# Performance work log

Hardware: AMD Instinct MI355X
Metric: run time of the kernel (lower is better)

The kernel has to match this reference:

```python
import jax, jax.numpy as jnp
import numpy as np
from jax import lax

L = 2        # encoder layers
D = 256      # d_model
H = 8        # nhead
DH = D // H  # head dim
CF = 2       # compression_factor (default in CustomizedAttn)
FF = 2048    # dim_feedforward
B = 10       # batch (forced: null_k has shape (10,1,D))
HH = 40
WW = 40
T = HH * WW  # seq len = 1600
EPS = 1e-5


def setup_inputs() -> dict:
    key = jax.random.key(0)
    ks = jax.random.split(key, 16)
    f = lambda k, shp: jax.random.normal(k, shp, jnp.float32) * 0.02
    return {
        "src": jax.random.normal(ks[0], (B, D, HH, WW), jnp.float32),
        "pos_embed": jax.random.normal(ks[1], (B, D, HH, WW), jnp.float32),
        "Wq": f(ks[2], (L, D, D)),
        "Wk": f(ks[3], (L, D, D)),
        "Wv": f(ks[4], (L, D, D)),
        "Wo": f(ks[5], (L, D, D)),
        "bo": jnp.zeros((L, D), jnp.float32),
        "conv_w": f(ks[6], (L, D, D // H, CF)),  # grouped Conv1d weight [out, in/groups, k]
        "conv_b": jnp.zeros((L, D), jnp.float32),
        "null_k": f(ks[7], (L, B, 1, D)),
        "null_v": f(ks[8], (L, B, 1, D)),
        "ln1_g": jnp.ones((L, D), jnp.float32),
        "ln1_b": jnp.zeros((L, D), jnp.float32),
        "ln2_g": jnp.ones((L, D), jnp.float32),
        "ln2_b": jnp.zeros((L, D), jnp.float32),
        "W1": f(ks[9], (L, FF, D)),
        "b1": jnp.zeros((L, FF), jnp.float32),
        "W2": f(ks[10], (L, D, FF)),
        "b2": jnp.zeros((L, D), jnp.float32),
    }


def _layernorm(x, g, b):
    m = jnp.mean(x, axis=-1, keepdims=True)
    v = jnp.var(x, axis=-1, keepdims=True)
    return (x - m) * lax.rsqrt(v + EPS) * g + b


def _attn(x, pos, Wq, Wk, Wv, Wo, bo, cw, cb, nk, nv):
    # x, pos: [B, T, D]
    qk = x + pos
    q = qk @ Wq.T
    k = qk @ Wk.T
    v = x @ Wv.T
    # torch: padding = cf - t % cf -> always in [1, cf], so padding ALWAYS applied
    pad = CF - (T % CF)
    k = jnp.pad(k, ((0, 0), (pad, 0), (0, 0)))
    v = jnp.pad(v, ((0, 0), (pad, 0), (0, 0)))

    def compress(t_):  # grouped strided Conv1d over time, shared weights for k and v
        y = lax.conv_general_dilated(
            t_.transpose(0, 2, 1), cw, (CF,), "VALID",
            dimension_numbers=("NCH", "OIH", "NCH"), feature_group_count=H)
        return (y + cb[None, :, None]).transpose(0, 2, 1)

    k = jnp.concatenate([nk, compress(k)], axis=1)  # [B, Tc+10, D]
    v = jnp.concatenate([nv, compress(v)], axis=1)
    split = lambda t_: t_.reshape(B, t_.shape[1], H, DH).transpose(0, 2, 1, 3)
    qh, kh, vh = split(q), split(k), split(v)
    # NOTE: scale uses FULL d_model (d ** -0.5), faithful to the source.
    dots = jnp.einsum("bhid,bhjd->bhij", qh, kh) * (D ** -0.5)
    # NOTE: the source computes softmax(dots) but then overwrites it with
    # dropout(dots); at inference attention weights are the raw scaled dots.
    out = jnp.einsum("bhij,bhjd->bhid", dots, vh)
    out = out.transpose(0, 2, 1, 3).reshape(B, T, D)
    return out @ Wo.T + bo


def reference(src, pos_embed, Wq, Wk, Wv, Wo, bo, conv_w, conv_b, null_k, null_v,
              ln1_g, ln1_b, ln2_g, ln2_b, W1, b1, W2, b2):
    x = src.reshape(B, D, T).transpose(0, 2, 1)        # [B, T, D]
    pos = pos_embed.reshape(B, D, T).transpose(0, 2, 1)
    for l in range(L):
        a = _attn(x, pos, Wq[l], Wk[l], Wv[l], Wo[l], bo[l],
                  conv_w[l], conv_b[l], null_k[l], null_v[l])
        x = _layernorm(x + a, ln1_g[l], ln1_b[l])
        ff = jnp.maximum(x @ W1[l].T + b1[l], 0.0) @ W2[l].T + b2[l]
        x = _layernorm(x + ff, ln2_g[l], ln2_b[l])
    return x.transpose(0, 2, 1).reshape(B, D, HH, WW)
```

## Files before the change

kernel.cpp:

```cpp
#include <hip/hip_runtime.h>
#include <math.h>

typedef __attribute__((ext_vector_type(8))) short short8;
typedef __attribute__((ext_vector_type(4))) short short4v;
typedef __attribute__((ext_vector_type(4))) float f32x4;
typedef unsigned int u32;

constexpr int Bsz = 10;
constexpr int Dm  = 256;
constexpr int Hh  = 8;
constexpr int Tt  = 1600;
constexpr int FFd = 2048;
constexpr int Tkv = 802;
constexpr int JCH = 8;
constexpr size_t Fsz  = (size_t)Bsz * Tt * Dm;
constexpr size_t PAD  = 65536;
constexpr size_t KVsz = (size_t)Bsz * Tkv * Dm;
constexpr size_t FHsz = (size_t)Bsz * Tt * FFd;
constexpr size_t WBsz = 2621440;

__device__ float g_x[Fsz];
__device__ float g_qk[Fsz];
__device__ float g_t[Fsz];
__device__ float g_kc[KVsz];
__device__ float g_vc[KVsz];
__device__ float g_kvm[(size_t)Bsz * Hh * 32 * 32];
__device__ float g_kvp[(size_t)JCH * Bsz * Hh * 32 * 32];
__device__ float g_pos[Fsz];
__device__ unsigned short g_xb[Fsz + PAD];
__device__ unsigned short g_qkb[Fsz + PAD];
__device__ unsigned short g_tb[Fsz + PAD];
__device__ unsigned short g_qb[Fsz + PAD];
__device__ __attribute__((aligned(16))) unsigned short g_ffh[FHsz + PAD];
__device__ unsigned short g_wb[WBsz];
__device__ unsigned short g_wo2[(size_t)Bsz * Dm * Dm];

__device__ __forceinline__ float* selbuf(int id) {
  switch (id) {
    case 0: return g_x;
    case 1: return g_qk;
    case 2: return g_t;
    case 3: return g_kc;
    case 4: return g_vc;
    case 5: return g_kvm;
    case 6: return (float*)g_ffh;
    default: return (float*)g_ffh + Fsz;
  }
}
__device__ __forceinline__ unsigned short* selbufb(int id) {
  switch (id) {
    case 0: return g_xb;
    case 1: return g_qkb;
    case 2: return g_tb;
    case 3: return g_ffh;
    default: return g_qb;
  }
}

__device__ __forceinline__ unsigned short f2b(float x) {
  unsigned int u = __float_as_uint(x);
  u += 0x7FFFu + ((u >> 16) & 1u);
  return (unsigned short)(u >> 16);
}
__device__ __forceinline__ float b2f(unsigned short u) {
  return __uint_as_float(((unsigned int)u) << 16);
}

__global__ __launch_bounds__(256) void wconv_all_k(
    const float* __restrict__ Wk, const float* __restrict__ Wq,
    const float* __restrict__ Wv, const float* __restrict__ Wo,
    const float* __restrict__ W1, const float* __restrict__ W2) {
  const int i = blockIdx.x * 256 + threadIdx.x;
  float v;
  if (i < 262144) {
    const int l = i >> 17, r = i & 131071;
    v = (r < 65536) ? Wk[l * 65536 + r] : Wq[l * 65536 + (r - 65536)];
  } else if (i < 393216) {
    v = Wv[i - 262144];
  } else if (i < 524288) {
    v = Wo[i - 393216];
  } else if (i < 1572864) {
    v = W1[i - 524288];
  } else {
    v = W2[i - 1572864];
  }
  g_wb[i] = f2b(v);
}

__global__ __launch_bounds__(256) void trans_in2_k(const float* __restrict__ src,
                                                   const float* __restrict__ pose) {
  __shared__ float ts[32][33];
  __shared__ float tp[32][33];
  const int tx = threadIdx.x & 31, ty = threadIdx.x >> 5;
  const int t0 = blockIdx.x * 32, d0 = blockIdx.y * 32, b = blockIdx.z;
  #pragma unroll
  for (int i = ty; i < 32; i += 8) {
    const size_t gi = ((size_t)(b * Dm + d0 + i)) * Tt + t0 + tx;
    ts[i][tx] = src[gi];
    tp[i][tx] = pose[gi];
  }
  __syncthreads();
  #pragma unroll
  for (int i = ty; i < 32; i += 8) {
    const size_t idx = ((size_t)(b * Tt + t0 + i)) * Dm + d0 + tx;
    const float s = ts[tx][i], p = tp[tx][i];
    g_x[idx] = s;
    g_pos[idx] = p;
    g_xb[idx] = f2b(s);
    g_qkb[idx] = f2b(s + p);
  }
}

__global__ __launch_bounds__(256) void trans_out_k(float* out) {
  __shared__ float tile[32][33];
  const int tx = threadIdx.x & 31, ty = threadIdx.x >> 5;
  const int t0 = blockIdx.x * 32, d0 = blockIdx.y * 32, b = blockIdx.z;
  #pragma unroll
  for (int i = ty; i < 32; i += 8)
    tile[i][tx] = g_x[((size_t)(b * Tt + t0 + i)) * Dm + d0 + tx];
  __syncthreads();
  #pragma unroll
  for (int i = ty; i < 32; i += 8)
    out[((size_t)(b * Dm + d0 + i)) * Tt + t0 + tx] = tile[tx][i];
}

template<int BN, bool DUAL, bool PERB, bool RELU, bool BIAS, bool CBF16>
__global__ __launch_bounds__(256) void gemm2_k(
    int Aid, int woff, const float* __restrict__ bias, int Cid, int C2id,
    int NB, int M, int N, int K) {
  constexpr int BM = 128, BK = 64;
  constexpr int ACH = BM * 8;
  constexpr int BCH = BN * 8;
  constexpr int NW = BN / 32;
  __shared__ short8 As8[3][ACH];
  __shared__ short8 Bs8[3][BCH];
  const int tid = threadIdx.x;
  const int lane = tid & 63, wid = tid >> 6;
  const int wr = wid >> 1, wc = wid & 1;

  const int nwg = gridDim.x;
  const int bid = blockIdx.x;
  const int q = nwg >> 3, r = nwg & 7;
  const int xcd = bid & 7, seq = bid >> 3;
  const int wgid = (xcd < r ? xcd * (q + 1) : r * (q + 1) + (xcd - r) * q) + seq;

  int m0, n0, mlim;
  const unsigned short* W16;
  if constexpr (PERB) {
    const int per = 13 * NB;
    const int b = wgid / per;
    const int rem = wgid - b * per;
    m0 = b * Tt + (rem / NB) * BM;
    n0 = (rem % NB) * BN;
    mlim = b * Tt + Tt;
    W16 = g_wo2 + (size_t)b * 65536;
  } else {
    m0 = (wgid / NB) * BM;
    n0 = (wgid % NB) * BN;
    mlim = M;
    W16 = g_wb + woff;
  }

  const unsigned short* A16 = selbufb(Aid);
  const bool second = DUAL && (n0 >= 256);
  float* Cf = selbuf(second ? C2id : Cid);
  unsigned short* C16 = selbufb(second ? C2id : Cid);
  const int gn0 = second ? n0 - 256 : n0;
  const int cstride = DUAL ? 256 : N;

  f32x4 acc[4][NW];
  #pragma unroll
  for (int m = 0; m < 4; ++m)
    #pragma unroll
    for (int n = 0; n < NW; ++n) acc[m][n] = (f32x4){0.f, 0.f, 0.f, 0.f};

  const int lkc = lane >> 4, lrc = lane & 15;

  auto stage = [&](int t, int buf) {
    const int k0 = t * BK;
    #pragma unroll
    for (int i = 0; i < ACH / 256; ++i) {
      const int c = tid + i * 256;
      const int row = c >> 3, kc = c & 7;
      const unsigned short* gs = A16 + (size_t)(m0 + row) * K + k0 +
                                 ((kc ^ (row & 7)) << 3);
      __builtin_amdgcn_global_load_lds(
          (const __attribute__((address_space(1))) u32*)gs,
          (__attribute__((address_space(3))) u32*)&As8[buf][c], 16, 0, 0);
    }
    #pragma unroll
    for (int i = 0; i < BCH / 256; ++i) {
      const int c = tid + i * 256;
      const int row = c >> 3, kc = c & 7;
      const unsigned short* gs = W16 + (size_t)(n0 + row) * K + k0 +
                                 ((kc ^ (row & 7)) << 3);
      __builtin_amdgcn_global_load_lds(
          (const __attribute__((address_space(1))) u32*)gs,
          (__attribute__((address_space(3))) u32*)&Bs8[buf][c], 16, 0, 0);
    }
  };

  const int nt = K / BK;
  stage(0, 0);
  if (nt > 1) stage(1, 1);
  int cur = 0, nxt = 2;
  for (int t = 0; t < nt; ++t) {
    if (t + 1 < nt) {
      asm volatile("s_waitcnt vmcnt(6)" ::: "memory");
    } else {
      asm volatile("s_waitcnt vmcnt(0)" ::: "memory");
    }
    __builtin_amdgcn_sched_barrier(0);
    __builtin_amdgcn_s_barrier();
    __builtin_amdgcn_sched_barrier(0);
    if (t + 2 < nt) stage(t + 2, nxt);
    #pragma unroll
    for (int kk = 0; kk < 2; ++kk) {
      short8 af[4], bf[NW];
      #pragma unroll
      for (int m = 0; m < 4; ++m) {
        const int r2 = wr * 64 + m * 16 + lrc;
        af[m] = As8[cur][r2 * 8 + ((kk * 4 + lkc) ^ (r2 & 7))];
      }
      #pragma unroll
      for (int n = 0; n < NW; ++n) {
        const int cn = wc * (BN / 2) + n * 16 + lrc;
        bf[n] = Bs8[cur][cn * 8 + ((kk * 4 + lkc) ^ (cn & 7))];
      }
      #pragma unroll
      for (int m = 0; m < 4; ++m)
        #pragma unroll
        for (int n = 0; n < NW; ++n)
          acc[m][n] = __builtin_amdgcn_mfma_f32_16x16x32_bf16(
              af[m], bf[n], acc[m][n], 0, 0, 0);
    }
    cur = (cur == 2) ? 0 : cur + 1;
    nxt = (nxt == 2) ? 0 : nxt + 1;
  }

  constexpr int CSTR = (BN == 64) ? BN + 4 : BN;
  float* ldsC = (float*)&As8[0][0];
  {
    asm volatile("s_waitcnt vmcnt(0)" ::: "memory");
    __builtin_amdgcn_s_barrier();
    const int r0 = lkc * 4;
    #pragma unroll
    for (int m = 0; m < 4; ++m)
      #pragma unroll
      for (int n = 0; n < NW; ++n) {
        const int col = wc * (BN / 2) + n * 16 + lrc;
        #pragma unroll
        for (int j = 0; j < 4; ++j)
          ldsC[(wr * 64 + m * 16 + r0 + j) * CSTR + col] = acc[m][n][j];
      }
    __syncthreads();
  }
  if constexpr (CBF16) {
    constexpr int CH = BM * BN / 8;
    #pragma unroll
    for (int i = 0; i < CH / 256; ++i) {
      const int c = tid + i * 256;
      const int rowl = c / (BN / 8), col8 = (c % (BN / 8)) * 8;
      if (PERB && m0 + rowl >= mlim) continue;
      short8 v;
      #pragma unroll
      for (int j = 0; j < 8; ++j) {
        float x = ldsC[rowl * CSTR + col8 + j];
        if (BIAS) x += bias[gn0 + col8 + j];
        if (RELU) x = fmaxf(x, 0.f);
        v[j] = (short)f2b(x);
      }
      *(short8*)(C16 + (size_t)(m0 + rowl) * cstride + gn0 + col8) = v;
    }
  } else {
    constexpr int CH = BM * BN / 4;
    #pragma unroll
    for (int i = 0; i < CH / 256; ++i) {
      const int c = tid + i * 256;
      const int rowl = c / (BN / 4), col4 = (c % (BN / 4)) * 4;
      if (PERB && m0 + rowl >= mlim) continue;
      float4 v;
      float* pv = &v.x;
      #pragma unroll
      for (int j = 0; j < 4; ++j) {
        float x = ldsC[rowl * CSTR + col4 + j];
        if (BIAS) x += bias[gn0 + col4 + j];
        if (RELU) x = fmaxf(x, 0.f);
        pv[j] = x;
      }
      *(float4*)(Cf + (size_t)(m0 + rowl) * cstride + gn0 + col4) = v;
    }
  }
}

__global__ __launch_bounds__(512, 1) void gemmf_k(
    int Aid, int w1off, int w2off, const float* __restrict__ b1p,
    const float* __restrict__ b2p) {
  constexpr int BM = 128, NCH = 16;
  __shared__ short8 ws[4096];
  __shared__ short8 h8[512];
  __shared__ float b1f[512];
  const int tid = threadIdx.x;
  const int lane = tid & 63, wid = tid >> 6;
  const int lkc = lane >> 4, lrc = lane & 15;
  const int nwg = gridDim.x, bid = blockIdx.x;
  const int q = nwg >> 3, r = nwg & 7;
  const int xcd = bid & 7, seq = bid >> 3;
  const int wgid = (xcd < r ? xcd * (q + 1) : r * (q + 1) + (xcd - r) * q) + seq;
  const int qd = wgid / 125;
  const int m0 = (wgid - qd * 125) * BM;
  const int hb = qd * 512;
  const unsigned short* A16 = selbufb(Aid);
  const unsigned short* W1p = g_wb + w1off;
  const unsigned short* W2p = g_wb + w2off;
  float* Cf;
  if (qd == 0) Cf = g_qk;
  else if (qd == 1) Cf = g_t;
  else Cf = (float*)g_ffh + (size_t)(qd - 2) * Fsz;

  #pragma unroll
  for (int i = 0; i < 8; ++i) {
    const int c = tid + i * 512;
    const int row = c >> 5, kc = c & 31;
    const unsigned short* gs = A16 + (size_t)(m0 + row) * 256 +
                               ((kc ^ (row & 31)) << 3);
    __builtin_amdgcn_global_load_lds(
        (const __attribute__((address_space(1))) u32*)gs,
        (__attribute__((address_space(3))) u32*)&ws[c], 16, 0, 0);
  }
  __builtin_amdgcn_global_load_lds(
      (const __attribute__((address_space(1))) u32*)(b1p + hb + tid),
      (__attribute__((address_space(3))) u32*)&b1f[tid], 4, 0, 0);
  asm volatile("s_waitcnt vmcnt(0)" ::: "memory");
  __builtin_amdgcn_sched_barrier(0);
  __builtin_amdgcn_s_barrier();

  const int mg = wid >> 1, ng = wid & 1;
  short8 areg[2][8];
  #pragma unroll
  for (int m = 0; m < 2; ++m)
    #pragma unroll
    for (int s = 0; s < 8; ++s) {
      const int r2 = mg * 32 + m * 16 + lrc;
      areg[m][s] = ws[r2 * 32 + ((s * 4 + lkc) ^ (r2 & 31))];
    }
  asm volatile("s_waitcnt lgkmcnt(0)" ::: "memory");
  __builtin_amdgcn_sched_barrier(0);
  __builtin_amdgcn_s_barrier();

  auto stage_w = [&](int ch, int buf) {
    const int kb = hb + ch * 32;
    #pragma unroll
    for (int i = 0; i < 2; ++i) {
      const int c = tid + i * 512;
      const int row = c >> 5, kc = c & 31;
      const unsigned short* gs = W1p + (size_t)(kb + row) * 256 +
                                 ((kc ^ (row & 31)) << 3);
      __builtin_amdgcn_global_load_lds(
          (const __attribute__((address_space(1))) u32*)gs,
          (__attribute__((address_space(3))) u32*)&ws[buf * 2048 + c], 16, 0, 0);
    }
    #pragma unroll
    for (int i = 0; i < 2; ++i) {
      const int c = tid + i * 512;
      const int row = c >> 2, kc = c & 3;
      const int g = (kc ^ (row & 3) ^ ((row >> 2) & 3)) & 3;
      const unsigned short* gs = W2p + (size_t)row * 2048 + kb + (g << 3);
      __builtin_amdgcn_global_load_lds(
          (const __attribute__((address_space(1))) u32*)gs,
          (__attribute__((address_space(3))) u32*)&ws[buf * 2048 + 1024 + c],
          16, 0, 0);
    }
  };
  stage_w(0, 0);

  const int wr = wid >> 2, wc = wid & 3;
  f32x4 acc2[4][4];
  #pragma unroll
  for (int m = 0; m < 4; ++m)
    #pragma unroll
    for (int n = 0; n < 4; ++n) acc2[m][n] = (f32x4){0.f, 0.f, 0.f, 0.f};

  for (int ch = 0; ch < NCH; ++ch) {
    const int cur = ch & 1;
    const int wb = cur * 2048;
    asm volatile("s_waitcnt vmcnt(0)" ::: "memory");
    __builtin_amdgcn_sched_barrier(0);
    __builtin_amdgcn_s_barrier();
    __builtin_amdgcn_sched_barrier(0);
    if (ch + 1 < NCH) stage_w(ch + 1, cur ^ 1);

    f32x4 a1[2];
    a1[0] = (f32x4){0.f, 0.f, 0.f, 0.f};
    a1[1] = (f32x4){0.f, 0.f, 0.f, 0.f};
    const int cn1 = ng * 16 + lrc;
    #pragma unroll
    for (int s = 0; s < 8; ++s) {
      short8 bf = ws[wb + cn1 * 32 + ((s * 4 + lkc) ^ cn1)];
      a1[0] = __builtin_amdgcn_mfma_f32_16x16x32_bf16(areg[0][s], bf, a1[0], 0, 0, 0);
      a1[1] = __builtin_amdgcn_mfma_f32_16x16x32_bf16(areg[1][s], bf, a1[1], 0, 0, 0);
    }
    unsigned short* h16 = (unsigned short*)h8;
    #pragma unroll
    for (int m = 0; m < 2; ++m)
      #pragma unroll
      for (int j = 0; j < 4; ++j) {
        const int row = mg * 32 + m * 16 + lkc * 4 + j;
        const float v = fmaxf(a1[m][j] + b1f[ch * 32 + cn1], 0.f);
        const int g = ((cn1 >> 3) ^ (row & 3) ^ ((row >> 2) & 3)) & 3;
        h16[row * 32 + g * 8 + (cn1 & 7)] = f2b(v);
      }
    asm volatile("s_waitcnt lgkmcnt(0)" ::: "memory");
    __builtin_amdgcn_sched_barrier(0);
    __builtin_amdgcn_s_barrier();
    __builtin_amdgcn_sched_barrier(0);

    short8 af2[4], bf2[4];
    #pragma unroll
    for (int m = 0; m < 4; ++m) {
      const int r2 = wr * 64 + m * 16 + lrc;
      af2[m] = h8[r2 * 4 + ((lkc ^ (r2 & 3) ^ ((r2 >> 2) & 3)) & 3)];
    }
    #pragma unroll
    for (int n = 0; n < 4; ++n) {
      const int cn = wc * 64 + n * 16 + lrc;
      bf2[n] = ws[wb + 1024 + cn * 4 + ((lkc ^ (cn & 3) ^ ((cn >> 2) & 3)) & 3)];
    }
    #pragma unroll
    for (int m = 0; m < 4; ++m)
      #pragma unroll
      for (int n = 0; n < 4; ++n)
        acc2[m][n] = __builtin_amdgcn_mfma_f32_16x16x32_bf16(
            af2[m], bf2[n], acc2[m][n], 0, 0, 0);
  }

  const int r0 = lkc * 4;
  #pragma unroll
  for (int m = 0; m < 4; ++m) {
    const int gm = m0 + wr * 64 + m * 16 + r0;
    #pragma unroll
    for (int n = 0; n < 4; ++n) {
      const int gn = wc * 64 + n * 16 + lrc;
      const float bb = (qd == 0) ? b2p[gn] : 0.f;
      #pragma unroll
      for (int j = 0; j < 4; ++j)
        Cf[(size_t)(gm + j) * 256 + gn] = acc2[m][n][j] + bb;
    }
  }
}

__global__ __launch_bounds__(256) void compress2_k(
    const float* __restrict__ cw, const float* __restrict__ cb,
    const float* __restrict__ nk, const float* __restrict__ nv) {
  __shared__ float rows[32][256];
  const int tc0 = 1 + blockIdx.x * 16;
  const int b = blockIdx.y;
  const int z = blockIdx.z;
  const int tid = threadIdx.x;
  const int o = tid;
  const int g = o >> 5;

  const unsigned short* srcbuf = z ? g_ffh : g_tb;
  const float* nul = z ? nv : nk;
  float* outb = (z ? g_vc : g_kc) + (size_t)b * Tkv * Dm;

  const int r0g = 2 * tc0 - 2;
  const unsigned short* src = srcbuf + ((size_t)b * Tt + r0g) * Dm;
  #pragma unroll
  for (int i = 0; i < 4; ++i) {
    const int c = tid + i * 256;
    const int row = c >> 5, off = (c & 31) * 8;
    short8 v = *(const short8*)(src + (size_t)row * 256 + off);
    #pragma unroll
    for (int j = 0; j < 8; ++j)
      rows[row][off + j] = b2f((unsigned short)v[j]);
  }

  float we[32], wo[32];
  {
    const float4* wp = (const float4*)(cw + o * 64);
    #pragma unroll
    for (int i = 0; i < 16; ++i) {
      float4 w4 = wp[i];
      we[i * 2 + 0] = w4.x; wo[i * 2 + 0] = w4.y;
      we[i * 2 + 1] = w4.z; wo[i * 2 + 1] = w4.w;
    }
  }
  const float bias = cb[o];
  if (blockIdx.x == 0) {
    outb[o] = nul[b * Dm + o];
    outb[Dm + o] = bias;
  }
  __syncthreads();

  float* outp = outb + o;
  #pragma unroll
  for (int t = 0; t < 16; ++t) {
    const int lr = 2 * t;
    const float* p0 = &rows[lr][g * 32];
    const float* p1 = &rows[lr + 1][g * 32];
    float acc = bias;
    #pragma unroll
    for (int i4 = 0; i4 < 8; ++i4) {
      float4 a0 = *(const float4*)(p0 + i4 * 4);
      float4 a1 = *(const float4*)(p1 + i4 * 4);
      acc = fmaf(we[i4 * 4 + 0], a0.x, acc);
      acc = fmaf(we[i4 * 4 + 1], a0.y, acc);
      acc = fmaf(we[i4 * 4 + 2], a0.z, acc);
      acc = fmaf(we[i4 * 4 + 3], a0.w, acc);
      acc = fmaf(wo[i4 * 4 + 0], a1.x, acc);
      acc = fmaf(wo[i4 * 4 + 1], a1.y, acc);
      acc = fmaf(wo[i4 * 4 + 2], a1.z, acc);
      acc = fmaf(wo[i4 * 4 + 3], a1.w, acc);
    }
    outp[(size_t)(1 + tc0 + t) * Dm] = acc;
  }
}

__global__ __launch_bounds__(256) void kvout1_k() {
  __shared__ float kl[8][32];
  __shared__ float vl[8][32];
  const int bh = blockIdx.x;
  const int js = blockIdx.y;
  const int b = bh >> 3, h = bh & 7;
  const int j0 = js * 101;
  const int jend = (j0 + 101 < Tkv) ? j0 + 101 : Tkv;

  const int tid = threadIdx.x;
  const int lr = tid >> 5;
  const int lc = tid & 31;
  const int e = tid >> 3;
  const int d0 = (tid & 7) * 4;

  float a0 = 0.f, a1 = 0.f, a2 = 0.f, a3 = 0.f;
  const size_t base = (size_t)b * Tkv * Dm + h * 32;

  for (int jc = j0; jc < jend; jc += 8) {
    const int jr = jc + lr;
    if (jr < jend) {
      kl[lr][lc] = g_kc[base + (size_t)jr * Dm + lc];
      vl[lr][lc] = g_vc[base + (size_t)jr * Dm + lc];
    } else {
      kl[lr][lc] = 0.f;
      vl[lr][lc] = 0.f;
    }
    __syncthreads();
    #pragma unroll
    for (int r = 0; r < 8; ++r) {
      const float kf = kl[r][e];
      const float* vr = &vl[r][d0];
      a0 = fmaf(kf, vr[0], a0);
      a1 = fmaf(kf, vr[1], a1);
      a2 = fmaf(kf, vr[2], a2);
      a3 = fmaf(kf, vr[3], a3);
    }
    __syncthreads();
  }
  float* op = g_kvp + ((size_t)js * 80 + bh) * 1024 + e * 32 + d0;
  op[0] = a0; op[1] = a1; op[2] = a2; op[3] = a3;
}

__global__ __launch_bounds__(256) void kvout2_k() {
  const int bh = blockIdx.x;
  const int tid = threadIdx.x;
  const int e = tid >> 3;
  const int d0 = (tid & 7) * 4;
  float a0 = 0.f, a1 = 0.f, a2 = 0.f, a3 = 0.f;
  #pragma unroll
  for (int s = 0; s < JCH; ++s) {
    const float* p = g_kvp + ((size_t)s * 80 + bh) * 1024 + e * 32 + d0;
    a0 += p[0]; a1 += p[1]; a2 += p[2]; a3 += p[3];
  }
  float* op = g_kvm + (size_t)bh * 1024 + e * 32 + d0;
  op[0] = a0 * 0.0625f;
  op[1] = a1 * 0.0625f;
  op[2] = a2 * 0.0625f;
  op[3] = a3 * 0.0625f;
}

__global__ __launch_bounds__(256) void wo2_k(int wooff) {
  const int n = blockIdx.x, b = blockIdx.y;
  const int he = threadIdx.x;
  const int h = he >> 5, e = he & 31;
  const float* kp = g_kvm + ((size_t)(b * Hh + h) * 32 + e) * 32;
  const unsigned short* wp = g_wb + wooff + (size_t)n * Dm + h * 32;
  float acc = 0.f;
  #pragma unroll
  for (int d = 0; d < 32; ++d) acc = fmaf(kp[d], b2f(wp[d]), acc);
  g_wo2[(size_t)b * 65536 + (size_t)n * Dm + he] = f2b(acc);
}

__global__ __launch_bounds__(256) void ln_k(int did, int did2, int did3,
                                            int did4, const float* g,
                                            const float* beta, int do_pos) {
  const int lane = threadIdx.x & 63;
  const int wave = threadIdx.x >> 6;
  const size_t row = (size_t)blockIdx.x * 4 + wave;
  float4 xv = ((const float4*)g_x)[row * 64 + lane];
  float4 dv = ((const float4*)selbuf(did))[row * 64 + lane];
  float v[4] = {xv.x + dv.x, xv.y + dv.y, xv.z + dv.z, xv.w + dv.w};
  if (did2 >= 0) {
    float4 d2 = ((const float4*)selbuf(did2))[row * 64 + lane];
    v[0] += d2.x; v[1] += d2.y; v[2] += d2.z; v[3] += d2.w;
  }
  if (did3 >= 0) {
    float4 d3 = ((const float4*)selbuf(did3))[row * 64 + lane];
    v[0] += d3.x; v[1] += d3.y; v[2] += d3.z; v[3] += d3.w;
  }
  if (did4 >= 0) {
    float4 d4 = ((const float4*)selbuf(did4))[row * 64 + lane];
    v[0] += d4.x; v[1] += d4.y; v[2] += d4.z; v[3] += d4.w;
  }
  float sum = v[0] + v[1] + v[2] + v[3];
  float sq = v[0]*v[0] + v[1]*v[1] + v[2]*v[2] + v[3]*v[3];
  #pragma unroll
  for (int off = 32; off; off >>= 1) {
    sum += __shfl_xor(sum, off);
    sq  += __shfl_xor(sq, off);
  }
  const float mean = sum * (1.f / 256.f);
  const float var = sq * (1.f / 256.f) - mean * mean;
  const float rs = rsqrtf(var + 1e-5f);
  float4 gg = ((const float4*)g)[lane];
  float4 bb = ((const float4*)beta)[lane];
  float4 ov;
  ov.x = (v[0] - mean) * rs * gg.x + bb.x;
  ov.y = (v[1] - mean) * rs * gg.y + bb.y;
  ov.z = (v[2] - mean) * rs * gg.z + bb.z;
  ov.w = (v[3] - mean) * rs * gg.w + bb.w;
  ((float4*)g_x)[row * 64 + lane] = ov;
  short4v sv;
  sv[0] = (short)f2b(ov.x); sv[1] = (short)f2b(ov.y);
  sv[2] = (short)f2b(ov.z); sv[3] = (short)f2b(ov.w);
  *(short4v*)&g_xb[(row * 64 + lane) * 4] = sv;
  if (do_pos) {
    float4 pv = ((const float4*)g_pos)[row * 64 + lane];
    short4v qv;
    qv[0] = (short)f2b(ov.x + pv.x); qv[1] = (short)f2b(ov.y + pv.y);
    qv[2] = (short)f2b(ov.z + pv.z); qv[3] = (short)f2b(ov.w + pv.w);
    *(short4v*)&g_qkb[(row * 64 + lane) * 4] = qv;
  }
}

extern "C" void kernel_launch(void* const* d_in, const int* in_sizes, int n_in,
                              void* d_out, int out_size, void* d_ws, size_t ws_size,
                              hipStream_t stream) {
  const float* src  = (const float*)d_in[0];
  const float* pose = (const float*)d_in[1];
  const float* Wq   = (const float*)d_in[2];
  const float* Wk   = (const float*)d_in[3];
  const float* Wv   = (const float*)d_in[4];
  const float* Wo   = (const float*)d_in[5];
  const float* bo   = (const float*)d_in[6];
  const float* cw   = (const float*)d_in[7];
  const float* cb   = (const float*)d_in[8];
  const float* nk   = (const float*)d_in[9];
  const float* nv   = (const float*)d_in[10];
  const float* ln1g = (const float*)d_in[11];
  const float* ln1b = (const float*)d_in[12];
  const float* ln2g = (const float*)d_in[13];
  const float* ln2b = (const float*)d_in[14];
  const float* W1   = (const float*)d_in[15];
  const float* b1   = (const float*)d_in[16];
  const float* W2   = (const float*)d_in[17];
  const float* b2   = (const float*)d_in[18];

  const int MT = Bsz * Tt;
  const dim3 tgrid(Tt / 32, Dm / 32, Bsz);

  const int OV = 262144, OO = 393216, O1 = 524288, O2 = 1572864;
  wconv_all_k<<<10240, 256, 0, stream>>>(Wk, Wq, Wv, Wo, W1, W2);
  trans_in2_k<<<tgrid, 256, 0, stream>>>(src, pose);

  const int MB = MT / 128;
  for (int l = 0; l < 2; ++l) {
    const float* bo_l = bo + (size_t)l * Dm;
    const float* cw_l = cw + (size_t)l * Dm * 64;
    const float* cb_l = cb + (size_t)l * Dm;
    const float* nk_l = nk + (size_t)l * Bsz * Dm;
    const float* nv_l = nv + (size_t)l * Bsz * Dm;
    const float* b1_l = b1 + (size_t)l * FFd;
    const float* b2_l = b2 + (size_t)l * Dm;
    const int wkq = l * 131072;
    const int wv = OV + l * 65536, wo = OO + l * 65536;
    const int w1 = O1 + l * 524288, w2 = O2 + l * 524288;

    gemm2_k<64, true, false, false, false, true><<<8 * MB, 256, 0, stream>>>(
        1, wkq, nullptr, 2, 4, 8, MT, 512, Dm);
    gemm2_k<64, false, false, false, false, true><<<4 * MB, 256, 0, stream>>>(
        0, wv, nullptr, 3, 3, 4, MT, Dm, Dm);
    compress2_k<<<dim3(50, Bsz, 2), 256, 0, stream>>>(cw_l, cb_l, nk_l, nv_l);
    kvout1_k<<<dim3(Bsz * Hh, JCH), 256, 0, stream>>>();
    kvout2_k<<<Bsz * Hh, 256, 0, stream>>>();
    wo2_k<<<dim3(Dm, Bsz), 256, 0, stream>>>(wo);
    gemm2_k<64, false, true, false, true, false><<<Bsz * 13 * 4, 256, 0, stream>>>(
        4, 0, bo_l, 2, 2, 4, MT, Dm, Dm);
    ln_k<<<MT / 4, 256, 0, stream>>>(2, -1, -1, -1,
                                     ln1g + l * Dm, ln1b + l * Dm, 0);

    gemmf_k<<<500, 512, 0, stream>>>(0, w1, w2, b1_l, b2_l);
    ln_k<<<MT / 4, 256, 0, stream>>>(1, 2, 6, 7,
                                     ln2g + l * Dm, ln2b + l * Dm,
                                     l == 0 ? 1 : 0);
  }

  trans_out_k<<<tgrid, 256, 0, stream>>>((float*)d_out);
}
```

Baseline: 362.1 us.

## Split fused FFN into two hidden-dim halves with 1024-thread blocks

The fused FFN kernel moves from four hidden-dim quarters over 500 blocks of 512 threads to two halves over 250 blocks of 1024 threads, each with 32 chunks. Each wave now does one 16-row MFMA tile per chunk instead of two. Only two partial outputs (g_qk, g_t) are written, so the layernorm reduction reads two partial sums instead of four, cutting intermediate memory traffic. The cost is fewer blocks (250 across 256 CUs), longer serial chunk loops per block, and less register-level reuse of W tiles per wave.

```diff
diff --git a/kernel.cpp b/kernel.cpp
--- a/kernel.cpp
+++ b/kernel.cpp
@@ -293,13 +293,13 @@
   }
 }
 
-__global__ __launch_bounds__(512, 1) void gemmf_k(
+__global__ __launch_bounds__(1024, 1) void gemmf_k(
     int Aid, int w1off, int w2off, const float* __restrict__ b1p,
     const float* __restrict__ b2p) {
-  constexpr int BM = 128, NCH = 16;
+  constexpr int BM = 128, NCH = 32;
   __shared__ short8 ws[4096];
   __shared__ short8 h8[512];
-  __shared__ float b1f[512];
+  __shared__ float b1f[1024];
   const int tid = threadIdx.x;
   const int lane = tid & 63, wid = tid >> 6;
   const int lkc = lane >> 4, lrc = lane & 15;
@@ -307,20 +307,17 @@
   const int q = nwg >> 3, r = nwg & 7;
   const int xcd = bid & 7, seq = bid >> 3;
   const int wgid = (xcd < r ? xcd * (q + 1) : r * (q + 1) + (xcd - r) * q) + seq;
-  const int qd = wgid / 125;
-  const int m0 = (wgid - qd * 125) * BM;
-  const int hb = qd * 512;
+  const int half = (wgid >= 125) ? 1 : 0;
+  const int m0 = (wgid - half * 125) * BM;
+  const int hb = half * 1024;
   const unsigned short* A16 = selbufb(Aid);
   const unsigned short* W1p = g_wb + w1off;
   const unsigned short* W2p = g_wb + w2off;
-  float* Cf;
-  if (qd == 0) Cf = g_qk;
-  else if (qd == 1) Cf = g_t;
-  else Cf = (float*)g_ffh + (size_t)(qd - 2) * Fsz;
-
-  #pragma unroll
-  for (int i = 0; i < 8; ++i) {
-    const int c = tid + i * 512;
+  float* Cf = half ? g_t : g_qk;
+
+  #pragma unroll
+  for (int i = 0; i < 4; ++i) {
+    const int c = tid + i * 1024;
     const int row = c >> 5, kc = c & 31;
     const unsigned short* gs = A16 + (size_t)(m0 + row) * 256 +
                                ((kc ^ (row & 31)) << 3);
@@ -336,23 +333,20 @@
   __builtin_amdgcn_s_barrier();
 
   const int mg = wid >> 1, ng = wid & 1;
-  short8 areg[2][8];
-  #pragma unroll
-  for (int m = 0; m < 2; ++m)
-    #pragma unroll
-    for (int s = 0; s < 8; ++s) {
-      const int r2 = mg * 32 + m * 16 + lrc;
-      areg[m][s] = ws[r2 * 32 + ((s * 4 + lkc) ^ (r2 & 31))];
-    }
+  short8 areg[8];
+  #pragma unroll
+  for (int s = 0; s < 8; ++s) {
+    const int r2 = mg * 16 + lrc;
+    areg[s] = ws[r2 * 32 + ((s * 4 + lkc) ^ (r2 & 31))];
+  }
   asm volatile("s_waitcnt lgkmcnt(0)" ::: "memory");
   __builtin_amdgcn_sched_barrier(0);
   __builtin_amdgcn_s_barrier();
 
   auto stage_w = [&](int ch, int buf) {
     const int kb = hb + ch * 32;
-    #pragma unroll
-    for (int i = 0; i < 2; ++i) {
-      const int c = tid + i * 512;
+    {
+      const int c = tid;
       const int row = c >> 5, kc = c & 31;
       const unsigned short* gs = W1p + (size_t)(kb + row) * 256 +
                                  ((kc ^ (row & 31)) << 3);
@@ -360,9 +354,8 @@
           (const __attribute__((address_space(1))) u32*)gs,
           (__attribute__((address_space(3))) u32*)&ws[buf * 2048 + c], 16, 0, 0);
     }
-    #pragma unroll
-    for (int i = 0; i < 2; ++i) {
-      const int c = tid + i * 512;
+    {
+      const int c = tid;
       const int row = c >> 2, kc = c & 3;
       const int g = (kc ^ (row & 3) ^ ((row >> 2) & 3)) & 3;
       const unsigned short* gs = W2p + (size_t)row * 2048 + kb + (g << 3);
@@ -375,9 +368,9 @@
   stage_w(0, 0);
 
   const int wr = wid >> 2, wc = wid & 3;
-  f32x4 acc2[4][4];
-  #pragma unroll
-  for (int m = 0; m < 4; ++m)
+  f32x4 acc2[2][4];
+  #pragma unroll
+  for (int m = 0; m < 2; ++m)
     #pragma unroll
     for (int n = 0; n < 4; ++n) acc2[m][n] = (f32x4){0.f, 0.f, 0.f, 0.f};
 
@@ -390,35 +383,30 @@
     __builtin_amdgcn_sched_barrier(0);
     if (ch + 1 < NCH) stage_w(ch + 1, cur ^ 1);
 
-    f32x4 a1[2];
-    a1[0] = (f32x4){0.f, 0.f, 0.f, 0.f};
-    a1[1] = (f32x4){0.f, 0.f, 0.f, 0.f};
+    f32x4 a1 = (f32x4){0.f, 0.f, 0.f, 0.f};
     const int cn1 = ng * 16 + lrc;
     #pragma unroll
     for (int s = 0; s < 8; ++s) {
       short8 bf = ws[wb + cn1 * 32 + ((s * 4 + lkc) ^ cn1)];
-      a1[0] = __builtin_amdgcn_mfma_f32_16x16x32_bf16(areg[0][s], bf, a1[0], 0, 0, 0);
-      a1[1] = __builtin_amdgcn_mfma_f32_16x16x32_bf16(areg[1][s], bf, a1[1], 0, 0, 0);
+      a1 = __builtin_amdgcn_mfma_f32_16x16x32_bf16(areg[s], bf, a1, 0, 0, 0);
     }
     unsigned short* h16 = (unsigned short*)h8;
     #pragma unroll
-    for (int m = 0; m < 2; ++m)
-      #pragma unroll
-      for (int j = 0; j < 4; ++j) {
-        const int row = mg * 32 + m * 16 + lkc * 4 + j;
-        const float v = fmaxf(a1[m][j] + b1f[ch * 32 + cn1], 0.f);
-        const int g = ((cn1 >> 3) ^ (row & 3) ^ ((row >> 2) & 3)) & 3;
-        h16[row * 32 + g * 8 + (cn1 & 7)] = f2b(v);
-      }
+    for (int j = 0; j < 4; ++j) {
+      const int row = mg * 16 + lkc * 4 + j;
+      const float v = fmaxf(a1[j] + b1f[ch * 32 + cn1], 0.f);
+      const int g = ((cn1 >> 3) ^ (row & 3) ^ ((row >> 2) & 3)) & 3;
+      h16[row * 32 + g * 8 + (cn1 & 7)] = f2b(v);
+    }
     asm volatile("s_waitcnt lgkmcnt(0)" ::: "memory");
     __builtin_amdgcn_sched_barrier(0);
     __builtin_amdgcn_s_barrier();
     __builtin_amdgcn_sched_barrier(0);
 
-    short8 af2[4], bf2[4];
-    #pragma unroll
-    for (int m = 0; m < 4; ++m) {
-      const int r2 = wr * 64 + m * 16 + lrc;
+    short8 af2[2], bf2[4];
+    #pragma unroll
+    for (int m = 0; m < 2; ++m) {
+      const int r2 = wr * 32 + m * 16 + lrc;
       af2[m] = h8[r2 * 4 + ((lkc ^ (r2 & 3) ^ ((r2 >> 2) & 3)) & 3)];
     }
     #pragma unroll
@@ -427,7 +415,7 @@
       bf2[n] = ws[wb + 1024 + cn * 4 + ((lkc ^ (cn & 3) ^ ((cn >> 2) & 3)) & 3)];
     }
     #pragma unroll
-    for (int m = 0; m < 4; ++m)
+    for (int m = 0; m < 2; ++m)
       #pragma unroll
       for (int n = 0; n < 4; ++n)
         acc2[m][n] = __builtin_amdgcn_mfma_f32_16x16x32_bf16(
@@ -436,12 +424,12 @@
 
   const int r0 = lkc * 4;
   #pragma unroll
-  for (int m = 0; m < 4; ++m) {
-    const int gm = m0 + wr * 64 + m * 16 + r0;
+  for (int m = 0; m < 2; ++m) {
+    const int gm = m0 + wr * 32 + m * 16 + r0;
     #pragma unroll
     for (int n = 0; n < 4; ++n) {
       const int gn = wc * 64 + n * 16 + lrc;
-      const float bb = (qd == 0) ? b2p[gn] : 0.f;
+      const float bb = (half == 0) ? b2p[gn] : 0.f;
       #pragma unroll
       for (int j = 0; j < 4; ++j)
         Cf[(size_t)(gm + j) * 256 + gn] = acc2[m][n][j] + bb;
@@ -698,8 +686,8 @@
     ln_k<<<MT / 4, 256, 0, stream>>>(2, -1, -1, -1,
                                      ln1g + l * Dm, ln1b + l * Dm, 0);
 
-    gemmf_k<<<500, 512, 0, stream>>>(0, w1, w2, b1_l, b2_l);
-    ln_k<<<MT / 4, 256, 0, stream>>>(1, 2, 6, 7,
+    gemmf_k<<<250, 1024, 0, stream>>>(0, w1, w2, b1_l, b2_l);
+    ln_k<<<MT / 4, 256, 0, stream>>>(1, 2, -1, -1,
                                      ln2g + l * Dm, ln2b + l * Dm,
                                      l == 0 ? 1 : 0);
   }
```

Result: faster. 334.1 us (-7.7%).
